# Kernel tuning notes

Hardware: AMD Instinct MI355X
Metric: run time of the kernel (lower is better)

The kernel has to match this reference:

```python
import jax, jax.numpy as jnp
import numpy as np
from math import factorial, pi

# ---- static module config (ModelEncodeDecodeSimple defaults) ----
B_IN, B_OUT = 30, 10        # input / output bandwidths
F_IN, F_OUT = 2, 5          # feature channels
BATCH = 512
N_ALPHA, MAX_BETA, N_BETA = 6, pi / 160.0, 1  # s2_near_identity_grid args


def _wigner_d(l, beta):
    """Wigner-d matrix d^l_{m',m}(beta), rows m'=-l..l, cols m=-l..l (quantum norm, CS phase)."""
    cb, sb = np.cos(beta / 2.0), np.sin(beta / 2.0)
    d = np.zeros((2 * l + 1, 2 * l + 1))
    for i, mp in enumerate(range(-l, l + 1)):
        for j, m in enumerate(range(-l, l + 1)):
            pref = np.sqrt(float(factorial(l + m) * factorial(l - m) * factorial(l + mp) * factorial(l - mp)))
            tot = 0.0
            for s in range(max(0, m - mp), min(l + m, l - mp) + 1):
                den = factorial(l + m - s) * factorial(s) * factorial(mp - m + s) * factorial(l - mp - s)
                tot += ((-1.0) ** (mp - m + s) / den) * cb ** (2 * l + m - mp - 2 * s) * sb ** (mp - m + 2 * s)
            d[i, j] = pref * tot
    return d


def _quad_weights(b):
    """Driscoll-Healy quadrature weights on the SOFT beta grid (lie_learn S2.quadrature_weights)."""
    k = np.arange(b)
    betas = pi * (2 * np.arange(2 * b) + 1) / (4 * b)
    return (2.0 / b) * np.sin(betas) * np.array(
        [np.sum(np.sin((2 * j + 1) * (2 * k + 1) * pi / (4 * b)) / (2 * k + 1)) for j in range(2 * b)])


# ---- precomputed constants (all static, numpy) ----
_betas_in = pi * (2 * np.arange(2 * B_IN) + 1) / (4 * B_IN)
_w = _quad_weights(B_IN)
NSPEC_S2 = B_OUT ** 2  # sum over l<b_out of (2l+1)
W_S2 = np.zeros((2 * B_IN, NSPEC_S2), dtype=np.float32)   # w_k * d^l_{m0}(beta_k)
FREQ_IN = np.zeros(NSPEC_S2, dtype=np.int64)              # alpha FFT bin for each (l,m)
for l in range(B_OUT):
    d_m0 = np.stack([_wigner_d(l, bb)[:, l] for bb in _betas_in])  # [2b_in, 2l+1]
    W_S2[:, l * l:l * l + 2 * l + 1] = (_w[:, None] * d_m0).astype(np.float32)
    FREQ_IN[l * l:l * l + 2 * l + 1] = np.arange(-l, l + 1) % (2 * B_IN)

# kernel grid: s2_near_identity_grid(n_alpha=6, max_beta=pi/160, n_beta=1)
_gb = np.arange(1, N_BETA + 1) * MAX_BETA / N_BETA
_ga = np.linspace(0, 2 * pi, N_ALPHA, endpoint=False)
GB, GA = np.meshgrid(_gb, _ga, indexing='ij')
GB, GA = GB.ravel(), GA.ravel()
N_GRID = GB.size
K_FT = np.zeros((NSPEC_S2, N_GRID), dtype=np.complex64)   # D^l_{m0}(alpha_g, beta_g, 0)
for l in range(B_OUT):
    for g in range(N_GRID):
        d_m0 = _wigner_d(l, GB[g])[:, l]
        K_FT[l * l:l * l + 2 * l + 1, g] = d_m0 * np.exp(-1j * np.arange(-l, l + 1) * GA[g])
SCALING = np.float32(1.0 / np.sqrt(N_GRID * F_IN * (B_OUT ** 4.0) / (B_IN ** 2.0)))

# SO(3) inverse-FFT Wigner blocks at output betas, scaled by (2l+1) (s2cnn so3_ifft convention)
_betas_out = pi * (2 * np.arange(2 * B_OUT) + 1) / (4 * B_OUT)
D_SO3 = [np.stack([_wigner_d(l, bb) for bb in _betas_out]).astype(np.float32) * (2 * l + 1)
         for l in range(B_OUT)]


def s2conv(x, kernel, bias):
    Bsz = x.shape[0]
    # --- S2 FFT of input: FFT over alpha, then quadrature-weighted Wigner contraction over beta ---
    Xf = jnp.fft.fft(x, axis=-1)                     # [B, f_in, 2b_in(beta), 2b_in(alpha-freq)] c64
    gx = Xf[:, :, :, FREQ_IN]                        # [B, f_in, 2b_in, nspec]
    fhat = jnp.einsum('bfks,ks->sbf', gx, W_S2.astype(np.complex64))   # [nspec, B, f_in]
    # --- kernel spherical FT on the near-identity grid ---
    yhat = jnp.einsum('iog,sg->sio', kernel * SCALING, K_FT)           # [nspec, f_in, f_out]
    # --- per-degree outer product (s2_mm, conj on kernel) + SO(3) spectral accumulation ---
    T = jnp.zeros((Bsz, F_OUT, 2 * B_OUT, 2 * B_OUT, 2 * B_OUT), dtype=fhat.dtype)
    for l in range(B_OUT):
        L = 2 * l + 1
        xl = fhat[l * l:l * l + L]                   # [L, B, f_in]
        yl = yhat[l * l:l * l + L]                   # [L, f_in, f_out]
        zl = jnp.einsum('mbi,nio->mnbo', xl, jnp.conj(yl))             # z^l_{mn}
        contrib = jnp.einsum('mnbo,kmn->bokmn', zl, D_SO3[l].astype(np.complex64))
        mi = np.arange(-l, l + 1) % (2 * B_OUT)
        T = T.at[:, :, :, mi[:, None], mi[None, :]].add(contrib)
    # --- inverse FFT over (alpha, gamma); SOFT convention multiplies by (2b)^2; take real part ---
    out = jnp.fft.ifft2(T, axes=(-2, -1)).real * float((2 * B_OUT) ** 2)
    return out + bias                                # [B, f_out, 2b_out, 2b_out, 2b_out]


def setup_inputs() -> dict:
    key = jax.random.key(0)
    k1, k2, k3 = jax.random.split(key, 3)
    x1 = jax.random.normal(k1, (BATCH, F_IN, 2 * B_IN, 2 * B_IN), dtype=jnp.float32)
    kernel = jax.random.normal(k2, (F_IN, F_OUT, N_GRID), dtype=jnp.float32)
    bias = jax.random.normal(k3, (1, F_OUT, 1, 1, 1), dtype=jnp.float32)
    return {"x1": x1, "kernel": kernel, "bias": bias}


def reference(x1, kernel, bias):
    return s2conv(x1, kernel, bias)
```

## Files before the change

kernel.cpp:

```cpp
#include <hip/hip_runtime.h>
#include <math.h>
#include <stdint.h>


typedef _Float16 half8 __attribute__((ext_vector_type(8)));
typedef float    f32x4 __attribute__((ext_vector_type(4)));

#define WS_W    128
#define WS_Y    17760
#define WS_EM   19776
#define WS_TRIG 20992
#define WS_PACK 21184
#define WS_AP   21952
#define WS_FH   107968
#define WS_DT   220608
#define WS_F    234908

#define IX_Y0    3300
#define IX_EM0   4300
#define IX_RT0   4900
#define IX_PACK0 5090
#define IX_AP0   5805
#define IX_DT0   177837
#define N_SETUP  192137

__device__ __forceinline__ double ipow_d(double x, int e) {
    double r = 1.0;
    for (int i = 0; i < e; ++i) r *= x;
    return r;
}

__device__ double dsmall(int l, int mp, int m, double beta) {
    double fact[20];
    fact[0] = 1.0;
    for (int i = 1; i < 20; ++i) fact[i] = fact[i - 1] * (double)i;
    double cb = cos(0.5 * beta), sb = sin(0.5 * beta);
    double pref = sqrt(fact[l + m] * fact[l - m] * fact[l + mp] * fact[l - mp]);
    int s0 = m - mp; if (s0 < 0) s0 = 0;
    int s1 = l + m;  if (l - mp < s1) s1 = l - mp;
    double tot = 0.0;
    for (int s = s0; s <= s1; ++s) {
        double den = fact[l + m - s] * fact[s] * fact[mp - m + s] * fact[l - mp - s];
        double sgn = ((mp - m + s) & 1) ? -1.0 : 1.0;
        tot += sgn / den * ipow_d(cb, 2 * l + m - mp - 2 * s) * ipow_d(sb, mp - m + 2 * s);
    }
    return pref * tot;
}

extern "C" __global__ void k_setup_w(float* wsf) {
    double* w = (double*)wsf;
    int t = threadIdx.x;
    if (t < 60) {
        double beta = M_PI * (2 * t + 1) / 120.0;
        double sum = 0.0;
        for (int k = 0; k < 30; ++k)
            sum += sin((double)((2 * t + 1) * (2 * k + 1)) * M_PI / 120.0) / (double)(2 * k + 1);
        w[t] = (2.0 / 30.0) * sin(beta) * sum;
    }
    if (t < 20) {
        double ang = M_PI * (double)t / 10.0;
        ((double*)(wsf + WS_TRIG))[t]      = sin(ang);
        ((double*)(wsf + WS_TRIG))[20 + t] = cos(ang);
    }
}

extern "C" __global__ void k_setup_const(float* wsf, const float* __restrict__ kern) {
    const double* w = (const double*)wsf;
    const int tri[11] = {0, 1, 3, 6, 10, 15, 21, 28, 36, 45, 55};
    int idx = blockIdx.x * 64 + threadIdx.x;
    if (idx < IX_Y0) {
        int k = idx / 55, smi = idx % 55;
        int l = 0; while (smi >= tri[l + 1]) ++l;
        int m = smi - tri[l];
        double beta = M_PI * (2 * k + 1) / 120.0;
        wsf[WS_W + idx] = (float)(w[k] * dsmall(l, m, 0, beta));
    } else if (idx < IX_EM0) {
        int i3 = idx - IX_Y0;
        int o = i3 / 200, r5 = i3 % 200;
        int s = r5 / 2, i = r5 % 2;
        int l = 0; while ((l + 1) * (l + 1) <= s) ++l;
        int n = s - l * l - l;
        double dv = dsmall(l, n, 0, M_PI / 160.0);
        const double SC = 1.0 / sqrt(6.0 * 2.0 * 10000.0 / 900.0);
        double ar = 0.0, ai = 0.0;
        for (int g = 0; g < 6; ++g) {
            double kv = (double)kern[i * 30 + o * 6 + g];
            double ang = (double)n * M_PI * (double)g / 3.0;
            ar += kv * cos(ang);
            ai -= kv * sin(ang);
        }
        ((float2*)(wsf + WS_Y))[i3] = make_float2((float)(SC * dv * ar), (float)(SC * dv * ai));
    } else if (idx < IX_RT0) {
        int t = idx - IX_EM0; int m = t / 60, j = t % 60;
        double a = 2.0 * M_PI * (double)(m * j) / 60.0;
        ((float2*)(wsf + WS_EM))[t] = make_float2((float)cos(a), (float)(-sin(a)));
    } else if (idx < IX_PACK0) {
    } else if (idx < IX_AP0) {
        int p = idx - IX_PACK0;
        int l = 0, bcur = 0;
        for (;;) { int bs = (l + 1) * (2 * l + 1); if (p < bcur + bs) break; bcur += bs; ++l; }
        int r = p - bcur; int L = 2 * l + 1;
        int m = r / L; int n = r % L - l;
        int smi = tri[l] + m; int sf = l * l + l + n;
        ((int*)(wsf + WS_PACK))[p] = smi * 128 + sf;
    } else if (idx < IX_DT0) {
        int ap = idx - IX_AP0;
        int j = ap & 7, lane = (ap >> 3) & 63, tc = ap >> 9;
        int t = tc % 28, c = tc / 28;
        int pq = t * 16 + (lane & 15);
        int kidx = c * 32 + ((lane >> 4) << 3) + j;
        double val = 0.0;
        if (pq < 400 && kidx < 380) {
            int r = kidx >> 1, cpart = kidx & 1;
            int m = r / 19, nn = r % 19, n = nn - 9;
            int p = pq / 20, q = pq % 20;
            int th = ((m * p + n * q) % 20 + 20) % 20;
            double wm = m ? 2.0 : 1.0;
            const double* st = (const double*)(wsf + WS_TRIG);
            val = cpart ? (-wm * st[th]) : (wm * st[20 + th]);
        }
        ((_Float16*)(wsf + WS_AP))[ap] = (_Float16)val;
    } else if (idx < N_SETUP) {
        int i6 = idx - IX_DT0;
        int p = i6 / 20, k = i6 % 20;
        int l = 0, bcur = 0;
        for (;;) { int bs = (l + 1) * (2 * l + 1); if (p < bcur + bs) break; bcur += bs; ++l; }
        int r = p - bcur; int L = 2 * l + 1;
        int m = r / L; int n = r % L - l;
        double beta = M_PI * (2 * k + 1) / 40.0;
        wsf[WS_DT + i6] = (float)((double)L * dsmall(l, m, n, beta));
    }
}

extern "C" __global__ void __launch_bounds__(256) k_fhat(const float* __restrict__ x,
                                                          float* __restrict__ wsf) {
    __shared__ float  xs[3600];
    __shared__ float2 ems[610];
    __shared__ float2 Y[600];
    int tid = threadIdx.x;
    int bi = blockIdx.x;
    const float4* xp = (const float4*)(x + bi * 3600);
    for (int t = tid; t < 900; t += 256) ((float4*)xs)[t] = xp[t];
    const float2* gEm = (const float2*)(wsf + WS_EM);
    for (int t = tid; t < 600; t += 256) {
        int m = t / 60, j = t - m * 60;
        ems[m * 61 + j] = gEm[t];
    }
    __syncthreads();
    for (int it = tid; it < 600; it += 256) {
        int k = it / 10, m = it - k * 10;
        const float*  row = xs + k * 60;
        const float2* em  = ems + m * 61;
        float ar = 0.f, ai = 0.f;
        #pragma unroll 12
        for (int j = 0; j < 60; ++j) {
            float xv = row[j];
            float2 e = em[j];
            ar += xv * e.x; ai += xv * e.y;
        }
        Y[it] = make_float2(ar, ai);
    }
    __syncthreads();
    if (tid < 55) {
        int smi = tid;
        const int tri[11] = {0, 1, 3, 6, 10, 15, 21, 28, 36, 45, 55};
        int l = 0; while (smi >= tri[l + 1]) ++l;
        int m = smi - tri[l];
        const float* gW = wsf + WS_W;
        float ar = 0.f, ai = 0.f;
        for (int kk = 0; kk < 60; ++kk) {
            float wv = gW[kk * 55 + smi];
            float2 y = Y[kk * 10 + m];
            ar += wv * y.x; ai += wv * y.y;
        }
        int b = bi >> 1, i = bi & 1;
        ((float2*)(wsf + WS_FH))[b * 110 + smi * 2 + i] = make_float2(ar, ai);
    }
}

template<int L>
__device__ __forceinline__ void fsum(int m, int n, int ko, const float* __restrict__ gDT,
                                     const float2* __restrict__ zp, float& fr, float& fi) {
    const int baseL[10] = {0, 1, 7, 22, 50, 95, 161, 252, 372, 525};
    float dv[10 - L];
    float2 zv[10 - L];
    #pragma unroll
    for (int l = L; l < 10; ++l) {
        int p = baseL[l] + m * (2 * l + 1) + n + l;
        dv[l - L] = gDT[p * 20 + ko];
        zv[l - L] = zp[p];
    }
    #pragma unroll
    for (int l = L; l < 10; ++l) {
        fr += dv[l - L] * zv[l - L].x;
        fi += dv[l - L] * zv[l - L].y;
    }
}

extern "C" __global__ void __launch_bounds__(256) k_zF(float* __restrict__ wsf) {
    __shared__ float2 zsh[2860];
    __shared__ float4 fbl4[110];
    __shared__ float4 yol4[500];
    int tid = threadIdx.x;
    int half = blockIdx.x & 1;
    int nb   = blockIdx.x >> 1;
    int n0 = nb * 64;
    int PO0 = n0 / 20;
    int bf = PO0 / 5;

    const float4* gfh4 = (const float4*)(wsf + WS_FH);
    for (int t = tid; t < 110; t += 256) {
        int bsel = t / 55, i55 = t - bsel * 55;
        int b = bf + bsel;
        fbl4[t] = (b < 512) ? gfh4[b * 55 + i55] : make_float4(0.f, 0.f, 0.f, 0.f);
    }
    for (int t = tid; t < 500; t += 256) yol4[t] = ((const float4*)(wsf + WS_Y))[t];
    __syncthreads();
    const int* gPack = (const int*)(wsf + WS_PACK);
    for (int pp = 0; pp < 4; ++pp) {
        int po = PO0 + pp;
        int b_loc = po / 5 - bf, o = po % 5;
        for (int p = tid; p < 715; p += 256) {
            int pk = gPack[p];
            int smi = pk >> 7, sf = pk & 127;
            float4 f = fbl4[b_loc * 55 + smi];
            float4 y = yol4[o * 100 + sf];
            float zr = f.x * y.x + f.y * y.y + f.z * y.z + f.w * y.w;
            float zi = f.y * y.x - f.x * y.y + f.w * y.z - f.z * y.w;
            zsh[pp * 715 + p] = make_float2(zr, zi);
        }
    }
    __syncthreads();

    int col = tid & 63;
    int ko  = (n0 + col) % 20;
    int pp  = ((n0 % 20) + col) / 20;
    int gg  = (n0 >> 4) + (col >> 4);
    int c15 = col & 15;
    const float* gDT = wsf + WS_DT;
    uint32_t*    gF  = (uint32_t*)(wsf + WS_F);
    const float2* zp = zsh + pp * 715;
    for (int it = tid; it < 6080; it += 256) {
        int r = __builtin_amdgcn_readfirstlane(((it >> 6) << 1) | half);
        int m = r / 19;
        int n = r - m * 19 - 9;
        int a = n < 0 ? -n : n;
        int lmin = m > a ? m : a;
        float fr = 0.f, fi = 0.f;
        switch (lmin) {
            case 0: fsum<0>(m, n, ko, gDT, zp, fr, fi); break;
            case 1: fsum<1>(m, n, ko, gDT, zp, fr, fi); break;
            case 2: fsum<2>(m, n, ko, gDT, zp, fr, fi); break;
            case 3: fsum<3>(m, n, ko, gDT, zp, fr, fi); break;
            case 4: fsum<4>(m, n, ko, gDT, zp, fr, fi); break;
            case 5: fsum<5>(m, n, ko, gDT, zp, fr, fi); break;
            case 6: fsum<6>(m, n, ko, gDT, zp, fr, fi); break;
            case 7: fsum<7>(m, n, ko, gDT, zp, fr, fi); break;
            case 8: fsum<8>(m, n, ko, gDT, zp, fr, fi); break;
            default: fsum<9>(m, n, ko, gDT, zp, fr, fi); break;
        }
        int chunk = r >> 4, w5 = (2 * r) & 31;
        int qp = w5 >> 3, dwi = (w5 & 7) >> 1;
        union { _Float16 h[2]; uint32_t u; } fv;
        fv.h[0] = (_Float16)fr; fv.h[1] = (_Float16)fi;
        gF[((chunk * 3200 + gg) * 64 + (qp * 16 + c15)) * 4 + dwi] = fv.u;
    }
    if (half == 0 && tid < 128) {
        int cc = tid >> 1, dwi = 2 + (tid & 1);
        int g2 = (n0 >> 4) + (cc >> 4);
        gF[((11 * 3200 + g2) * 64 + (48 + (cc & 15))) * 4 + dwi] = 0u;
    }
}

extern "C" __global__ void __launch_bounds__(256) k_gemm2(const float* __restrict__ wsf,
                                                           const float* __restrict__ bias,
                                                           float* __restrict__ out) {
    int tid = threadIdx.x;
    int h  = blockIdx.x & 1;
    int n0 = (blockIdx.x >> 1) * 64;
    int wave = tid >> 6, lane = tid & 63;
    int g0 = n0 >> 4;
    const half8* gA = (const half8*)(wsf + WS_AP);
    const half8* gB = (const half8*)(wsf + WS_F);
    int nt = (h == 0 && wave == 0) ? 4 : 3;
    int t0 = h * 13 + (h == 0 ? (wave == 0 ? 0 : 4 + 3 * (wave - 1)) : 3 * wave);

    f32x4 acc[4][4];
    #pragma unroll
    for (int tt = 0; tt < 4; ++tt)
        #pragma unroll
        for (int f = 0; f < 4; ++f) acc[tt][f] = (f32x4){0.f, 0.f, 0.f, 0.f};

    half8 bufB[2][4], bufA[2][4];
    #pragma unroll
    for (int f = 0; f < 4; ++f) bufB[0][f] = gB[(g0 + f) * 64 + lane];
    #pragma unroll
    for (int tt = 0; tt < 4; ++tt)
        if (tt < nt) bufA[0][tt] = gA[(t0 + tt) * 64 + lane];

    #pragma unroll
    for (int c = 0; c < 12; ++c) {
        const int cur = c & 1, nxt = cur ^ 1;
        if (c < 11) {
            #pragma unroll
            for (int f = 0; f < 4; ++f)
                bufB[nxt][f] = gB[((c + 1) * 3200 + g0 + f) * 64 + lane];
            #pragma unroll
            for (int tt = 0; tt < 4; ++tt)
                if (tt < nt) bufA[nxt][tt] = gA[((c + 1) * 28 + t0 + tt) * 64 + lane];
        }
        #pragma unroll
        for (int tt = 0; tt < 4; ++tt) {
            if (tt < nt) {
                #pragma unroll
                for (int f = 0; f < 4; ++f)
                    acc[tt][f] = __builtin_amdgcn_mfma_f32_16x16x32_f16(bufA[cur][tt], bufB[cur][f], acc[tt][f], 0, 0, 0);
            }
        }
    }

    int quad4 = (lane >> 4) << 2, col15 = lane & 15;
    float bo_f[4];
    #pragma unroll
    for (int f = 0; f < 4; ++f) bo_f[f] = bias[((n0 + f * 16 + col15) / 20) % 5];
    #pragma unroll
    for (int tt = 0; tt < 4; ++tt) {
        if (tt < nt) {
            int pqb = (t0 + tt) * 16 + quad4;
            #pragma unroll
            for (int f = 0; f < 4; ++f) {
                int n = n0 + f * 16 + col15;
                float bo = bo_f[f];
                float4 v = make_float4(acc[tt][f].x + bo, acc[tt][f].y + bo,
                                       acc[tt][f].z + bo, acc[tt][f].w + bo);
                *(float4*)(out + n * 400 + pqb) = v;
            }
        }
    }
}

extern "C" void kernel_launch(void* const* d_in, const int* in_sizes, int n_in,
                              void* d_out, int out_size, void* d_ws, size_t ws_size,
                              hipStream_t stream) {
    const float* x    = (const float*)d_in[0];
    const float* kern = (const float*)d_in[1];
    const float* bias = (const float*)d_in[2];
    float* out = (float*)d_out;
    float* wsf = (float*)d_ws;
    k_setup_w    <<<1,    64,  0, stream>>>(wsf);
    k_setup_const<<<3003, 64,  0, stream>>>(wsf, kern);
    k_fhat       <<<1024, 256, 0, stream>>>(x, wsf);
    k_zF         <<<1600, 256, 0, stream>>>(wsf);
    k_gemm2      <<<1600, 256, 0, stream>>>(wsf, bias, out);
}
```

Before: 187.9 us.

## Stage GEMM B tiles in LDS cooperatively and store z in fp16

In k_gemm2, the four waves now load all 12 B chunks into shared memory together, split across waves, instead of each wave redundantly fetching the same B tiles from global memory. The MFMA loop then reads B from LDS. This removes 4x redundant global traffic but adds 48 KB of LDS and a barrier, which can lower occupancy. Separately, k_zF packs the z intermediate as fp16 pairs in LDS, halving its footprint and read bandwidth at some precision cost.

```diff
diff --git a/kernel.cpp b/kernel.cpp
--- a/kernel.cpp
+++ b/kernel.cpp
@@ -180,10 +180,10 @@
 
 template<int L>
 __device__ __forceinline__ void fsum(int m, int n, int ko, const float* __restrict__ gDT,
-                                     const float2* __restrict__ zp, float& fr, float& fi) {
+                                     const uint32_t* zp, float& fr, float& fi) {
     const int baseL[10] = {0, 1, 7, 22, 50, 95, 161, 252, 372, 525};
     float dv[10 - L];
-    float2 zv[10 - L];
+    uint32_t zv[10 - L];
     #pragma unroll
     for (int l = L; l < 10; ++l) {
         int p = baseL[l] + m * (2 * l + 1) + n + l;
@@ -192,13 +192,14 @@
     }
     #pragma unroll
     for (int l = L; l < 10; ++l) {
-        fr += dv[l - L] * zv[l - L].x;
-        fi += dv[l - L] * zv[l - L].y;
+        union { uint32_t u; _Float16 h[2]; } zc; zc.u = zv[l - L];
+        fr += dv[l - L] * (float)zc.h[0];
+        fi += dv[l - L] * (float)zc.h[1];
     }
 }
 
 extern "C" __global__ void __launch_bounds__(256) k_zF(float* __restrict__ wsf) {
-    __shared__ float2 zsh[2860];
+    __shared__ uint32_t zsh[2860];
     __shared__ float4 fbl4[110];
     __shared__ float4 yol4[500];
     int tid = threadIdx.x;
@@ -227,7 +228,9 @@
             float4 y = yol4[o * 100 + sf];
             float zr = f.x * y.x + f.y * y.y + f.z * y.z + f.w * y.w;
             float zi = f.y * y.x - f.x * y.y + f.w * y.z - f.z * y.w;
-            zsh[pp * 715 + p] = make_float2(zr, zi);
+            union { _Float16 h[2]; uint32_t u; } cv;
+            cv.h[0] = (_Float16)zr; cv.h[1] = (_Float16)zi;
+            zsh[pp * 715 + p] = cv.u;
         }
     }
     __syncthreads();
@@ -239,7 +242,7 @@
     int c15 = col & 15;
     const float* gDT = wsf + WS_DT;
     uint32_t*    gF  = (uint32_t*)(wsf + WS_F);
-    const float2* zp = zsh + pp * 715;
+    const uint32_t* zp = zsh + pp * 715;
     for (int it = tid; it < 6080; it += 256) {
         int r = __builtin_amdgcn_readfirstlane(((it >> 6) << 1) | half);
         int m = r / 19;
@@ -275,6 +278,7 @@
 extern "C" __global__ void __launch_bounds__(256) k_gemm2(const float* __restrict__ wsf,
                                                            const float* __restrict__ bias,
                                                            float* __restrict__ out) {
+    __shared__ __align__(16) _Float16 Bsh[12 * 4 * 64 * 8];
     int tid = threadIdx.x;
     int h  = blockIdx.x & 1;
     int n0 = (blockIdx.x >> 1) * 64;
@@ -282,6 +286,19 @@
     int g0 = n0 >> 4;
     const half8* gA = (const half8*)(wsf + WS_AP);
     const half8* gB = (const half8*)(wsf + WS_F);
+    half8* lB = (half8*)Bsh;
+
+    half8 stg[12];
+    #pragma unroll
+    for (int i = 0; i < 12; ++i) {
+        int cf = wave * 12 + i;
+        int c = cf >> 2, f = cf & 3;
+        stg[i] = gB[(c * 3200 + g0 + f) * 64 + lane];
+    }
+    #pragma unroll
+    for (int i = 0; i < 12; ++i)
+        lB[(wave * 12 + i) * 64 + lane] = stg[i];
+
     int nt = (h == 0 && wave == 0) ? 4 : 3;
     int t0 = h * 13 + (h == 0 ? (wave == 0 ? 0 : 4 + 3 * (wave - 1)) : 3 * wave);
 
@@ -291,30 +308,30 @@
         #pragma unroll
         for (int f = 0; f < 4; ++f) acc[tt][f] = (f32x4){0.f, 0.f, 0.f, 0.f};
 
-    half8 bufB[2][4], bufA[2][4];
-    #pragma unroll
-    for (int f = 0; f < 4; ++f) bufB[0][f] = gB[(g0 + f) * 64 + lane];
+    half8 bufA[2][4];
     #pragma unroll
     for (int tt = 0; tt < 4; ++tt)
         if (tt < nt) bufA[0][tt] = gA[(t0 + tt) * 64 + lane];
+
+    __syncthreads();
 
     #pragma unroll
     for (int c = 0; c < 12; ++c) {
         const int cur = c & 1, nxt = cur ^ 1;
         if (c < 11) {
             #pragma unroll
-            for (int f = 0; f < 4; ++f)
-                bufB[nxt][f] = gB[((c + 1) * 3200 + g0 + f) * 64 + lane];
-            #pragma unroll
             for (int tt = 0; tt < 4; ++tt)
                 if (tt < nt) bufA[nxt][tt] = gA[((c + 1) * 28 + t0 + tt) * 64 + lane];
         }
+        half8 bB[4];
+        #pragma unroll
+        for (int f = 0; f < 4; ++f) bB[f] = lB[(c * 4 + f) * 64 + lane];
         #pragma unroll
         for (int tt = 0; tt < 4; ++tt) {
             if (tt < nt) {
                 #pragma unroll
                 for (int f = 0; f < 4; ++f)
-                    acc[tt][f] = __builtin_amdgcn_mfma_f32_16x16x32_f16(bufA[cur][tt], bufB[cur][f], acc[tt][f], 0, 0, 0);
+                    acc[tt][f] = __builtin_amdgcn_mfma_f32_16x16x32_f16(bufA[cur][tt], bB[f], acc[tt][f], 0, 0, 0);
             }
         }
     }
```

Result: faster. 182.2 us (-3.1%).
